# Kernel optimization log

Measured on AMD Instinct MI355X. Metric: run time of the kernel, lower is better.

## Reference

```python
import jax, jax.numpy as jnp
import numpy as np
import math

B, L, D, H = 8, 1000, 1024, 16
HD = D // H

def setup_inputs() -> dict:
    key = jax.random.key(0)
    k1, k2, k3 = jax.random.split(key, 3)
    s_in = 1.0 / math.sqrt(D)
    x = jax.random.normal(k1, (B, L, D), dtype=jnp.float32)
    Wqkv = jax.random.normal(k2, (D, 3 * D), dtype=jnp.float32) * s_in
    bqkv = jnp.zeros((3 * D,), dtype=jnp.float32)
    Wo = jax.random.normal(k3, (D, D), dtype=jnp.float32) * s_in
    bo = jnp.zeros((D,), dtype=jnp.float32)
    return {"x": x, "Wqkv": Wqkv, "bqkv": bqkv, "Wo": Wo, "bo": bo}

def reference(x, Wqkv, bqkv, Wo, bo):
    b, l, d = x.shape
    qkv = x @ Wqkv + bqkv                      # [B,L,3D]
    q, k, v = jnp.split(qkv, 3, axis=-1)       # each [B,L,D]
    q = q.reshape(b, l, H, HD)
    k = k.reshape(b, l, H, HD)
    v = v.reshape(b, l, H, HD)
    scale = 1.0 / math.sqrt(HD)
    att = jnp.einsum('blhd,bmhd->bhlm', q, k) * scale   # [B,H,L,L]
    causal = jnp.tril(jnp.ones((l, l), dtype=bool))      # [L,L]
    att = jnp.where(causal[None, None, :, :], att, -jnp.inf)
    att = jax.nn.softmax(att, axis=-1)
    out = jnp.einsum('bhlm,bmhd->blhd', att, v).reshape(b, l, d)
    return out @ Wo + bo
```

## Files before the change

kernel.cpp:

```cpp
#include <hip/hip_runtime.h>
#include <hip/hip_bf16.h>

typedef unsigned short u16;
typedef unsigned int u32;
typedef __attribute__((ext_vector_type(8))) __bf16 bf16x8;
typedef __attribute__((ext_vector_type(4))) float f32x4;
typedef __attribute__((ext_vector_type(4))) u16 u16x4;

#define LQ 1000
#define MM 8000

__device__ __forceinline__ u16 f2bf(float f){
  __bf16 h = (__bf16)f;
  return __builtin_bit_cast(u16, h);
}
__device__ __forceinline__ void async_copy16(const void* g, void* l){
  __builtin_amdgcn_global_load_lds((const __attribute__((address_space(1))) u32*)g,
                                   (__attribute__((address_space(3))) u32*)l, 16, 0, 0);
}

__device__ __forceinline__ void ttile(const float* __restrict__ src, u16* __restrict__ dst,
                                      int R, int C, int bxt, int byt, u16 (*tile)[33]){
  const int tx = threadIdx.x & 31, ty = threadIdx.x >> 5;
  const long bx = (long)bxt * 32, by = (long)byt * 32;
  #pragma unroll
  for (int i = 0; i < 32; i += 8) tile[ty + i][tx] = f2bf(src[(by + ty + i) * C + bx + tx]);
  __syncthreads();
  #pragma unroll
  for (int i = 0; i < 32; i += 8) dst[(bx + ty + i) * R + by + tx] = tile[tx][ty + i];
}

__global__ __launch_bounds__(256)
void kprep(const float* __restrict__ x, u16* __restrict__ xb,
           const float* __restrict__ Wqkv, u16* __restrict__ WqkvT,
           const float* __restrict__ Wo, u16* __restrict__ WoT)
{
  __shared__ u16 tile[32][33];
  const int bid = blockIdx.x;
  if (bid < 2048) {
    const int t = threadIdx.x;
    for (long base = (long)bid * 1024; base < 8192000L; base += 2048L * 1024) {
      const long i = base + t * 4;
      const float4 v = *(const float4*)&x[i];
      u16x4 o; o.x = f2bf(v.x); o.y = f2bf(v.y); o.z = f2bf(v.z); o.w = f2bf(v.w);
      *(u16x4*)&xb[i] = o;
    }
  } else if (bid < 5120) {
    const int idx = bid - 2048;
    ttile(Wqkv, WqkvT, 1024, 3072, idx % 96, idx / 96, tile);
  } else {
    const int idx = bid - 5120;
    ttile(Wo, WoT, 1024, 1024, idx % 32, idx / 32, tile);
  }
}

template<int EPI, int BN>
__global__ __launch_bounds__(256)
void gemm128(const u16* __restrict__ A, const u16* __restrict__ BT, const float* __restrict__ bias,
             u16* __restrict__ O0, u16* __restrict__ O1, u16* __restrict__ O2,
             float* __restrict__ OF)
{
  constexpr int K = 1024;
  constexpr int NF = BN / 32;
  constexpr int NWGX = (EPI == 0) ? 24 : 8;
  constexpr int NWG  = NWGX * 63;
  __shared__ __align__(16) u16 As[2][128 * 32];
  __shared__ __align__(16) u16 Bs[2][BN * 32];
  const int t = threadIdx.x, lane = t & 63, wave = t >> 6;
  const int quad = lane >> 4, l15 = lane & 15;
  int lin = blockIdx.y * NWGX + blockIdx.x;
  lin = (lin & 7) * (NWG >> 3) + (lin >> 3);
  const int m0 = (lin / NWGX) * 128, n0 = (lin % NWGX) * BN;
  const int wm = (wave >> 1) * 64, wn = (wave & 1) * (BN / 2);

  f32x4 acc[4][NF] = {};

  const int srow = t >> 2;
  const int sg   = (t & 3) ^ ((srow >> 1) & 3);
  const int scol = sg * 8;
  const long aoff0 = (long)min(m0 + srow,      MM - 1) * K + scol;
  const long aoff1 = (long)min(m0 + srow + 64, MM - 1) * K + scol;
  const long boff0 = (long)(n0 + srow)      * K + scol;
  const long boff1 = (long)(n0 + srow + 64) * K + scol;
  char* AsB0 = (char*)As[0] + wave * 1024;
  char* AsB1 = (char*)As[1] + wave * 1024;
  char* BsB0 = (char*)Bs[0] + wave * 1024;
  char* BsB1 = (char*)Bs[1] + wave * 1024;

  const int swz = (l15 >> 1) & 3;

  for (int kt = 0; kt < K; kt += 64) {
    __syncthreads();
    async_copy16(A  + aoff0 + kt,      AsB0);
    async_copy16(A  + aoff1 + kt,      AsB0 + 4096);
    async_copy16(BT + boff0 + kt,      BsB0);
    if constexpr (BN == 128) async_copy16(BT + boff1 + kt,      BsB0 + 4096);
    async_copy16(A  + aoff0 + kt + 32, AsB1);
    async_copy16(A  + aoff1 + kt + 32, AsB1 + 4096);
    async_copy16(BT + boff0 + kt + 32, BsB1);
    if constexpr (BN == 128) async_copy16(BT + boff1 + kt + 32, BsB1 + 4096);
    __syncthreads();
    #pragma unroll
    for (int half = 0; half < 2; half++) {
      bf16x8 af[4], bfv[NF];
      #pragma unroll
      for (int i = 0; i < 4; i++)  af[i]  = *(const bf16x8*)&As[half][(wm + i * 16 + l15) * 32 + (quad ^ swz) * 8];
      #pragma unroll
      for (int i = 0; i < NF; i++) bfv[i] = *(const bf16x8*)&Bs[half][(wn + i * 16 + l15) * 32 + (quad ^ swz) * 8];
      #pragma unroll
      for (int mi = 0; mi < 4; mi++)
        #pragma unroll
        for (int ni = 0; ni < NF; ni++)
          acc[mi][ni] = __builtin_amdgcn_mfma_f32_16x16x32_bf16(af[mi], bfv[ni], acc[mi][ni], 0, 0, 0);
    }
  }

  float bs[NF]; int cols[NF];
  #pragma unroll
  for (int ni = 0; ni < NF; ni++) { cols[ni] = n0 + wn + ni * 16 + l15; bs[ni] = bias[cols[ni]]; }

  #pragma unroll
  for (int mi = 0; mi < 4; mi++) {
    #pragma unroll
    for (int r = 0; r < 4; r++) {
      const int row = m0 + wm + mi * 16 + quad * 4 + r;
      if (row >= MM) continue;
      if (EPI == 0) {
        const int b = row / 1000, l = row - b * 1000;
        #pragma unroll
        for (int ni = 0; ni < NF; ni++) {
          const u16 o = f2bf(acc[mi][ni][r] + bs[ni]);
          const int col = cols[ni];
          const int which = col >> 10, hh = (col >> 6) & 15, dd = col & 63;
          const int bh = b * 16 + hh;
          if      (which == 0) O0[((long)bh * LQ + l) * 64 + dd] = o;
          else if (which == 1) O1[((long)bh * LQ + l) * 64 + dd] = o;
          else                 O2[((long)bh * 64 + dd) * LQ + l] = o;
        }
      } else {
        #pragma unroll
        for (int ni = 0; ni < NF; ni++)
          OF[(long)row * 1024 + cols[ni]] = acc[mi][ni][r] + bs[ni];
      }
    }
  }
}

__global__ __launch_bounds__(256)
void attn_kernel(const u16* __restrict__ Qb, const u16* __restrict__ Kb,
                 const u16* __restrict__ VTb, u16* __restrict__ AO)
{
  __shared__ __align__(16) u16 Ps[4][2][16 * 40];
  const int t = threadIdx.x, lane = t & 63, wave = t >> 6;
  const int quad = lane >> 4, l15 = lane & 15;
  const int lin = blockIdx.y * 4 + blockIdx.x;
  const int swz = (lin & 7) * 64 + (lin >> 3);
  const int bh  = swz >> 2;
  const int s   = swz & 3;
  const int c   = ((wave & 2) ? 8 : 0) + ((wave & 1) ? (7 - s) : s);
  const int ch[2] = { c, 31 - c };
  const int nkt = 32 - c;
  const u16* Q  = Qb  + (long)bh * LQ * 64;
  const u16* Kp = Kb  + (long)bh * LQ * 64;
  const u16* VT = VTb + (long)bh * 64 * LQ;
  const int b = bh >> 4, h = bh & 15;
  const float sscale = 0.18033688011112042f;

  int qv[2][2]; bf16x8 bq0[2][2], bq1[2][2];
  #pragma unroll
  for (int cj = 0; cj < 2; cj++) {
    #pragma unroll
    for (int g = 0; g < 2; g++) {
      qv[cj][g] = ch[cj] * 32 + g * 16 + l15;
      const int qc = min(qv[cj][g], LQ - 1);
      bq0[cj][g] = *(const bf16x8*)&Q[(long)qc * 64 +      quad * 8];
      bq1[cj][g] = *(const bf16x8*)&Q[(long)qc * 64 + 32 + quad * 8];
    }
  }

  float l_p[2][2] = {{0.f, 0.f}, {0.f, 0.f}};
  f32x4 o[2][2][4] = {};

  bf16x8 pa00, pa01, pa10, pa11, pav0, pav1, pav2, pav3;
  {
    const int krA = min(l15, LQ - 1), krB = min(16 + l15, LQ - 1);
    pa00 = *(const bf16x8*)&Kp[(long)krA * 64 +      quad * 8];
    pa01 = *(const bf16x8*)&Kp[(long)krA * 64 + 32 + quad * 8];
    pa10 = *(const bf16x8*)&Kp[(long)krB * 64 +      quad * 8];
    pa11 = *(const bf16x8*)&Kp[(long)krB * 64 + 32 + quad * 8];
    const int vcol = min(quad * 8, LQ - 8);
    pav0 = *(const bf16x8*)&VT[(long)( 0 + l15) * LQ + vcol];
    pav1 = *(const bf16x8*)&VT[(long)(16 + l15) * LQ + vcol];
    pav2 = *(const bf16x8*)&VT[(long)(32 + l15) * LQ + vcol];
    pav3 = *(const bf16x8*)&VT[(long)(48 + l15) * LQ + vcol];
  }

  for (int kk = 0; kk < nkt; ++kk) {
    const int k0 = kk * 32;
    const bf16x8 a00 = pa00, a01 = pa01, a10 = pa10, a11 = pa11;
    bf16x8 av[4] = { pav0, pav1, pav2, pav3 };
    if (kk + 1 < nkt) {
      const int n0k = k0 + 32;
      const int krA = min(n0k + l15, LQ - 1), krB = min(n0k + 16 + l15, LQ - 1);
      pa00 = *(const bf16x8*)&Kp[(long)krA * 64 +      quad * 8];
      pa01 = *(const bf16x8*)&Kp[(long)krA * 64 + 32 + quad * 8];
      pa10 = *(const bf16x8*)&Kp[(long)krB * 64 +      quad * 8];
      pa11 = *(const bf16x8*)&Kp[(long)krB * 64 + 32 + quad * 8];
      const int vcol = min(n0k + quad * 8, LQ - 8);
      pav0 = *(const bf16x8*)&VT[(long)( 0 + l15) * LQ + vcol];
      pav1 = *(const bf16x8*)&VT[(long)(16 + l15) * LQ + vcol];
      pav2 = *(const bf16x8*)&VT[(long)(32 + l15) * LQ + vcol];
      pav3 = *(const bf16x8*)&VT[(long)(48 + l15) * LQ + vcol];
    }

    #pragma unroll
    for (int cj = 0; cj < 2; cj++) {
      if (cj == 0 && kk > ch[0]) continue;
      const bool lastt = (kk == ch[cj]);
      #pragma unroll
      for (int g = 0; g < 2; g++) {
        const f32x4 z = {};
        __builtin_amdgcn_s_setprio(1);
        f32x4 s0 = __builtin_amdgcn_mfma_f32_16x16x32_bf16(a00, bq0[cj][g], z, 0, 0, 0);
        s0       = __builtin_amdgcn_mfma_f32_16x16x32_bf16(a01, bq1[cj][g], s0, 0, 0, 0);
        f32x4 s1 = __builtin_amdgcn_mfma_f32_16x16x32_bf16(a10, bq0[cj][g], z, 0, 0, 0);
        s1       = __builtin_amdgcn_mfma_f32_16x16x32_bf16(a11, bq1[cj][g], s1, 0, 0, 0);
        __builtin_amdgcn_s_setprio(0);

        float p0[4], p1[4];
        if (lastt) {
          const int q = qv[cj][g];
          #pragma unroll
          for (int r = 0; r < 4; r++) {
            const int key0 = k0 + quad * 4 + r;
            p0[r] = __builtin_amdgcn_exp2f((key0      <= q) ? s0[r] * sscale : -3.0e38f);
            p1[r] = __builtin_amdgcn_exp2f((key0 + 16 <= q) ? s1[r] * sscale : -3.0e38f);
          }
        } else {
          #pragma unroll
          for (int r = 0; r < 4; r++) {
            p0[r] = __builtin_amdgcn_exp2f(s0[r] * sscale);
            p1[r] = __builtin_amdgcn_exp2f(s1[r] * sscale);
          }
        }
        u16x4 w0, w1; float ls = 0.f;
        #pragma unroll
        for (int r = 0; r < 4; r++) {
          w0[r] = f2bf(p0[r]); w1[r] = f2bf(p1[r]);
          ls += p0[r] + p1[r];
        }
        l_p[cj][g] += ls;
        *(u16x4*)&Ps[wave][g][l15 * 40 + quad * 4]      = w0;
        *(u16x4*)&Ps[wave][g][l15 * 40 + 16 + quad * 4] = w1;
        const bf16x8 bp = *(const bf16x8*)&Ps[wave][g][l15 * 40 + quad * 8];
        __builtin_amdgcn_s_setprio(1);
        #pragma unroll
        for (int cc = 0; cc < 4; cc++)
          o[cj][g][cc] = __builtin_amdgcn_mfma_f32_16x16x32_bf16(av[cc], bp, o[cj][g][cc], 0, 0, 0);
        __builtin_amdgcn_s_setprio(0);
      }
    }
  }

  #pragma unroll
  for (int cj = 0; cj < 2; cj++) {
    #pragma unroll
    for (int g = 0; g < 2; g++) {
      if (qv[cj][g] >= LQ) continue;
      float l = l_p[cj][g];
      l += __shfl_xor(l, 16);
      l += __shfl_xor(l, 32);
      const float inv = 1.0f / l;
      const long base = ((long)(b * LQ + qv[cj][g])) * 1024 + h * 64;
      #pragma unroll
      for (int cc = 0; cc < 4; cc++) {
        u16x4 w;
        #pragma unroll
        for (int r = 0; r < 4; r++) w[r] = f2bf(o[cj][g][cc][r] * inv);
        *(u16x4*)&AO[base + cc * 16 + quad * 4] = w;
      }
    }
  }
}

extern "C" void kernel_launch(void* const* d_in, const int* in_sizes, int n_in,
                              void* d_out, int out_size, void* d_ws, size_t ws_size,
                              hipStream_t stream) {
  const float* x    = (const float*)d_in[0];
  const float* Wqkv = (const float*)d_in[1];
  const float* bqkv = (const float*)d_in[2];
  const float* Wo   = (const float*)d_in[3];
  const float* bo   = (const float*)d_in[4];
  float* out = (float*)d_out;

  char* ws = (char*)d_ws;
  u16* WqkvT = (u16*)(ws);
  u16* WoT   = (u16*)(ws + 6291456);
  u16* xb    = (u16*)(ws + 8388608);
  u16* Qb    = (u16*)(ws + 8388608 + 16384000L);
  u16* Kb    = (u16*)(ws + 8388608 + 2 * 16384000L);
  u16* VTb   = (u16*)(ws + 8388608 + 3 * 16384000L);
  u16* AO    = xb;

  kprep<<<6144, 256, 0, stream>>>(x, xb, Wqkv, WqkvT, Wo, WoT);
  gemm128<0, 128><<<dim3(24, 63), 256, 0, stream>>>(xb, WqkvT, bqkv, Qb, Kb, VTb, nullptr);
  attn_kernel<<<dim3(4, 128), 256, 0, stream>>>(Qb, Kb, VTb, AO);
  gemm128<1, 128><<<dim3(8, 63), 256, 0, stream>>>(AO, WoT, bo, nullptr, nullptr, nullptr, out);
}
```

Measured before the change: 243.1 us.

## Software-pipeline GEMM K-loop with double-buffered async LDS prefetch

```diff
diff --git a/kernel.cpp b/kernel.cpp
--- a/kernel.cpp
+++ b/kernel.cpp
@@ -61,6 +61,7 @@
              float* __restrict__ OF)
 {
   constexpr int K = 1024;
+  constexpr int NC = K / 32;
   constexpr int NF = BN / 32;
   constexpr int NWGX = (EPI == 0) ? 24 : 8;
   constexpr int NWG  = NWGX * 63;
@@ -82,37 +83,37 @@
   const long aoff1 = (long)min(m0 + srow + 64, MM - 1) * K + scol;
   const long boff0 = (long)(n0 + srow)      * K + scol;
   const long boff1 = (long)(n0 + srow + 64) * K + scol;
-  char* AsB0 = (char*)As[0] + wave * 1024;
-  char* AsB1 = (char*)As[1] + wave * 1024;
-  char* BsB0 = (char*)Bs[0] + wave * 1024;
-  char* BsB1 = (char*)Bs[1] + wave * 1024;
 
   const int swz = (l15 >> 1) & 3;
 
-  for (int kt = 0; kt < K; kt += 64) {
+  auto STAGE = [&](int c, int b){
+    const long ko = (long)c * 32;
+    char* Ad = (char*)As[b] + wave * 1024;
+    char* Bd = (char*)Bs[b] + wave * 1024;
+    async_copy16(A  + aoff0 + ko, Ad);
+    async_copy16(A  + aoff1 + ko, Ad + 4096);
+    async_copy16(BT + boff0 + ko, Bd);
+    if constexpr (BN == 128) async_copy16(BT + boff1 + ko, Bd + 4096);
+  };
+
+  STAGE(0, 0);
+
+  #pragma unroll 2
+  for (int c = 0; c < NC; ++c) {
     __syncthreads();
-    async_copy16(A  + aoff0 + kt,      AsB0);
-    async_copy16(A  + aoff1 + kt,      AsB0 + 4096);
-    async_copy16(BT + boff0 + kt,      BsB0);
-    if constexpr (BN == 128) async_copy16(BT + boff1 + kt,      BsB0 + 4096);
-    async_copy16(A  + aoff0 + kt + 32, AsB1);
-    async_copy16(A  + aoff1 + kt + 32, AsB1 + 4096);
-    async_copy16(BT + boff0 + kt + 32, BsB1);
-    if constexpr (BN == 128) async_copy16(BT + boff1 + kt + 32, BsB1 + 4096);
-    __syncthreads();
-    #pragma unroll
-    for (int half = 0; half < 2; half++) {
-      bf16x8 af[4], bfv[NF];
+    if (c + 1 < NC) STAGE(c + 1, (c + 1) & 1);
+    const u16* Ab = As[c & 1];
+    const u16* Bb = Bs[c & 1];
+    bf16x8 af[4], bfv[NF];
+    #pragma unroll
+    for (int i = 0; i < 4; i++)  af[i]  = *(const bf16x8*)&Ab[(wm + i * 16 + l15) * 32 + (quad ^ swz) * 8];
+    #pragma unroll
+    for (int i = 0; i < NF; i++) bfv[i] = *(const bf16x8*)&Bb[(wn + i * 16 + l15) * 32 + (quad ^ swz) * 8];
+    #pragma unroll
+    for (int mi = 0; mi < 4; mi++)
       #pragma unroll
-      for (int i = 0; i < 4; i++)  af[i]  = *(const bf16x8*)&As[half][(wm + i * 16 + l15) * 32 + (quad ^ swz) * 8];
-      #pragma unroll
-      for (int i = 0; i < NF; i++) bfv[i] = *(const bf16x8*)&Bs[half][(wn + i * 16 + l15) * 32 + (quad ^ swz) * 8];
-      #pragma unroll
-      for (int mi = 0; mi < 4; mi++)
-        #pragma unroll
-        for (int ni = 0; ni < NF; ni++)
-          acc[mi][ni] = __builtin_amdgcn_mfma_f32_16x16x32_bf16(af[mi], bfv[ni], acc[mi][ni], 0, 0, 0);
-    }
+      for (int ni = 0; ni < NF; ni++)
+        acc[mi][ni] = __builtin_amdgcn_mfma_f32_16x16x32_bf16(af[mi], bfv[ni], acc[mi][ni], 0, 0, 0);
   }
 
   float bs[NF]; int cols[NF];
```

Result: slower. 252.5 us (+3.9%).
